# Kernel tuning notes

Hardware: AMD Instinct MI355X
Metric: run time of the kernel (lower is better)

Reference implementation:

```python
import jax, jax.numpy as jnp
import numpy as np

N_NODES = 100_000
N_EDGES = 1_600_000
N_GRAPHS = 64
EPS = 1e-7  # GENConv message epsilon
D_IN, D_H, D_OUT, OUT_DIM = 128, 192, 128, 10


def _w(k, fan_in, fan_out):
    return jax.random.normal(k, (fan_in, fan_out), jnp.float32) * (1.0 / np.sqrt(fan_in))


def setup_inputs() -> dict:
    key = jax.random.key(0)
    ks = jax.random.split(key, 8)
    return {
        "x": jax.random.normal(ks[0], (N_NODES, D_IN), jnp.float32),
        "W0": _w(ks[1], D_IN, D_H), "b0": jnp.zeros((D_H,), jnp.float32),
        "W1": _w(ks[2], D_H, D_H), "b1": jnp.zeros((D_H,), jnp.float32),
        "W2": _w(ks[3], D_H, D_H), "b2": jnp.zeros((D_H,), jnp.float32),
        "W3": _w(ks[4], D_H, D_OUT), "b3": jnp.zeros((D_OUT,), jnp.float32),
        "Wfc": _w(ks[5], D_OUT, OUT_DIM), "bfc": jnp.zeros((OUT_DIM,), jnp.float32),
        "edge_index": jax.random.randint(ks[6], (2, N_EDGES), 0, N_NODES, jnp.int32),
        "batch": jnp.sort(jax.random.randint(ks[7], (N_NODES,), 0, N_GRAPHS, jnp.int32)),
    }


def _genconv(x, W, b, src, dst):
    # GENConv (num_layers=1, aggr='add'): message = relu(x_j) + eps,
    # scatter-add to dst, residual add, single Linear MLP.
    msg = jax.nn.relu(x[src]) + EPS          # [E, d]
    agg = jax.ops.segment_sum(msg, dst, num_segments=N_NODES)  # [N, d]
    return (x + agg) @ W + b


def reference(x, W0, b0, W1, b1, W2, b2, W3, b3, Wfc, bfc, edge_index, batch):
    src, dst = edge_index[0], edge_index[1]  # source_to_target flow
    for W, b in ((W0, b0), (W1, b1), (W2, b2), (W3, b3)):
        x = _genconv(x, W, b, src, dst)
    # global mean pool over graphs
    sums = jax.ops.segment_sum(x, batch, num_segments=N_GRAPHS)
    counts = jax.ops.segment_sum(jnp.ones((x.shape[0],), x.dtype), batch,
                                 num_segments=N_GRAPHS)
    pooled = sums / jnp.maximum(counts, 1.0)[:, None]  # [G, D_OUT]
    logits = pooled @ Wfc + bfc                        # [G, OUT_DIM]
    return jax.nn.log_softmax(logits, axis=1)
```

## Files before the change

kernel.cpp:

```cpp
#include <hip/hip_runtime.h>
#include <hip/hip_bf16.h>
#include <stdint.h>

constexpr int NN = 100000;
constexpr int NE = 1600000;
constexpr int NG = 64;
constexpr int S  = 192;
constexpr int NB_SCAN = 98;
constexpr unsigned int ZOFF = (unsigned int)NN * 384u;

constexpr int PREP_CONVX_BLK = 12500;
constexpr int PREP_INDEG_BLK = 1563;
constexpr int PREP_CONVW_BLK = 384;
constexpr int PREP_GB_BLK    = 391;
constexpr int PREP_GRID = PREP_CONVX_BLK + PREP_INDEG_BLK + PREP_CONVW_BLK + PREP_GB_BLK;

constexpr int EG_BLOCKS = 391;
constexpr int HROW = 50048;
constexpr int QROW = HROW / 4;

typedef __bf16 bf16x8 __attribute__((ext_vector_type(8)));
typedef float  f32x16 __attribute__((ext_vector_type(16)));
typedef float  f32x2  __attribute__((ext_vector_type(2)));

union U16x4 { uint4 u; bf16x8 b; };

__device__ __forceinline__ float bl(unsigned int u) { return __uint_as_float(u << 16); }
__device__ __forceinline__ float bh(unsigned int u) { return __uint_as_float(u & 0xffff0000u); }
__device__ __forceinline__ float b16f(unsigned short u) { return __uint_as_float(((unsigned int)u) << 16); }
__device__ __forceinline__ unsigned int fb(float f) {
    unsigned int u = __float_as_uint(f);
    return (u + 0x7fffu + ((u >> 16) & 1u)) >> 16;
}
__device__ __forceinline__ unsigned int prelu(unsigned int u) {
    unsigned int r;
    asm("v_pk_max_f16 %0, %1, %2" : "=v"(r) : "v"(u), "v"(0u));
    return r;
}
__device__ __forceinline__ unsigned int cnt2bf(unsigned int h) {
    float f0 = (float)(h & 0xffffu);
    float f1 = (float)(h >> 16);
    return (__float_as_uint(f0) >> 16) | (__float_as_uint(f1) & 0xffff0000u);
}

__global__ __launch_bounds__(256) void k_prep(const float* __restrict__ x,
                                              const int* __restrict__ ei,
                                              const int* __restrict__ bat,
                                              const float* __restrict__ W0, const float* __restrict__ W1,
                                              const float* __restrict__ W2,
                                              unsigned short* __restrict__ A_,
                                              int* __restrict__ indeg, int* __restrict__ slot,
                                              unsigned short* __restrict__ T0, unsigned short* __restrict__ T1,
                                              unsigned short* __restrict__ T2,
                                              int* __restrict__ nstart) {
    const int b = blockIdx.x;
    if (b < PREP_CONVX_BLK) {
        int id = b * 256 + threadIdx.x;
        if (id < 96) ((unsigned int*)(A_ + (size_t)NN * S))[id] = 0u;
        int row = id >> 5, c4 = id & 31;
        float4 v = ((const float4*)x)[id];
        uint2 a;
        a.x = fb(v.x) | (fb(v.y) << 16);
        a.y = fb(v.z) | (fb(v.w) << 16);
        *(uint2*)(A_ + row * S + c4 * 4) = a;
    } else if (b < PREP_CONVX_BLK + PREP_INDEG_BLK) {
        int e4 = ((b - PREP_CONVX_BLK) * 256 + threadIdx.x) * 4;
        if (e4 < NE) {
            int4 d = *(const int4*)(ei + NE + e4);
            int4 sl;
            sl.x = atomicAdd(&indeg[d.x], 1);
            sl.y = atomicAdd(&indeg[d.y], 1);
            sl.z = atomicAdd(&indeg[d.z], 1);
            sl.w = atomicAdd(&indeg[d.w], 1);
            *(int4*)(slot + e4) = sl;
        }
    } else if (b < PREP_CONVX_BLK + PREP_INDEG_BLK + PREP_CONVW_BLK) {
        int id = (b - PREP_CONVX_BLK - PREP_INDEG_BLK) * 256 + threadIdx.x;
        const float* W; unsigned short* T; int N, base;
        if      (id < 24576) { W = W0; T = T0; N = 192; base = 0;     }
        else if (id < 61440) { W = W1; T = T1; N = 192; base = 24576; }
        else                 { W = W2; T = T2; N = 192; base = 61440; }
        int lid = id - base;
        int ci = lid >> 3, j = lid & 7;
        int kc = ci / N, n = ci % N;
        T[lid] = (unsigned short)fb(W[(kc * 8 + j) * N + n]);
    } else {
        int n = (b - PREP_CONVX_BLK - PREP_INDEG_BLK - PREP_CONVW_BLK) * 256 + threadIdx.x;
        if (n < NN) {
            int b0 = bat[n];
            int bprev = (n == 0) ? -1 : bat[n - 1];
            for (int g = bprev + 1; g <= b0; g++) nstart[g] = n;
            if (n == NN - 1)
                for (int g = b0 + 1; g < NG; g++) nstart[g] = NN;
        }
    }
}

__global__ __launch_bounds__(1024) void k_scan1(const int* __restrict__ indeg, int* __restrict__ offs,
                                                int* __restrict__ partials) {
    __shared__ int s[1024];
    int t = threadIdx.x;
    int gid = blockIdx.x * 1024 + t;
    int v = (gid < NN) ? indeg[gid] : 0;
    s[t] = v;
    __syncthreads();
    for (int d = 1; d < 1024; d <<= 1) {
        int tv = (t >= d) ? s[t - d] : 0;
        __syncthreads();
        s[t] += tv;
        __syncthreads();
    }
    if (gid < NN) offs[gid + 1] = s[t];
    if (t == 1023) partials[blockIdx.x] = s[1023];
}

__global__ __launch_bounds__(128) void k_scan2(int* __restrict__ offs, int* __restrict__ partials) {
    __shared__ int s[128];
    int t = threadIdx.x;
    int v = (t < NB_SCAN) ? partials[t] : 0;
    s[t] = v;
    __syncthreads();
    for (int d = 1; d < 128; d <<= 1) {
        int tv = (t >= d) ? s[t - d] : 0;
        __syncthreads();
        s[t] += tv;
        __syncthreads();
    }
    if (t < NB_SCAN) partials[t] = s[t] - v;
    if (t == 0) offs[0] = 0;
}

__device__ __forceinline__ int toff(const int* __restrict__ offs, const int* __restrict__ part, int j) {
    return j ? (offs[j] + part[(j - 1) >> 10]) : 0;
}

__global__ __launch_bounds__(256) void k_fill(const int* __restrict__ ei, const int* __restrict__ offs,
                                              const int* __restrict__ part,
                                              const int* __restrict__ slot, int* __restrict__ csr) {
    int e4 = (blockIdx.x * 256 + threadIdx.x) * 4;
    if (e4 >= NE) return;
    int4 sv = *(const int4*)(ei + e4);
    int4 dv = *(const int4*)(ei + NE + e4);
    int4 sl = *(const int4*)(slot + e4);
    csr[toff(offs, part, dv.x) + sl.x] = sv.x;
    csr[toff(offs, part, dv.y) + sl.y] = sv.y;
    csr[toff(offs, part, dv.z) + sl.z] = sv.z;
    csr[toff(offs, part, dv.w) + sl.w] = sv.w;
}

__global__ __launch_bounds__(256, 8) void k_agg192(const unsigned short* __restrict__ Ain,
                                                   unsigned short* __restrict__ Yout,
                                                   const int* __restrict__ offs,
                                                   const int* __restrict__ part,
                                                   const int* __restrict__ indeg,
                                                   const int* __restrict__ csr) {
    const int w = threadIdx.x >> 6, lane = threadIdx.x & 63;
    const int i = __builtin_amdgcn_readfirstlane(blockIdx.x * 4 + w);
    const bool act = lane < 48;
    const int deg   = __builtin_amdgcn_readfirstlane(indeg[i]);
    const int start = __builtin_amdgcn_readfirstlane(toff(offs, part, i));
    const int fo = (act ? lane : 47) * 8;
    const char* Ab = (const char*)Ain;

    f32x2 A01, A23;
    {
        uint2 p = *(const uint2*)(Ab + (size_t)i * 384 + fo);
        const float ed = 1e-7f * (float)deg;
        A01 = (f32x2){bl(p.x) + ed, bh(p.x) + ed};
        A23 = (f32x2){bl(p.y) + ed, bh(p.y) + ed};
    }

    const int* ecsr = csr + start;
    for (int e = 0; e < deg; e += 16) {
        unsigned int off[16];
#pragma unroll
        for (int k = 0; k < 16; k++) {
            int v = ecsr[e + k];
            off[k] = (e + k < deg) ? (unsigned int)v * 384u : ZOFF;
        }
        uint2 p[16];
#pragma unroll
        for (int k = 0; k < 16; k++)
            p[k] = *(const uint2*)(Ab + (size_t)off[k] + fo);
#pragma unroll
        for (int k = 0; k < 16; k++) {
            unsigned int rx = prelu(p[k].x), ry = prelu(p[k].y);
            A01 += (f32x2){bl(rx), bh(rx)};
            A23 += (f32x2){bl(ry), bh(ry)};
        }
    }
    if (act) {
        uint2 o;
        o.x = fb(A01.x) | (fb(A01.y) << 16);
        o.y = fb(A23.x) | (fb(A23.y) << 16);
        *(uint2*)(Yout + (size_t)i * S + lane * 4) = o;
    }
}

__global__ __launch_bounds__(256, 8) void k_agg128(const unsigned short* __restrict__ Ain,
                                                   unsigned short* __restrict__ Yout,
                                                   const int* __restrict__ offs,
                                                   const int* __restrict__ part,
                                                   const int* __restrict__ indeg,
                                                   const int* __restrict__ csr) {
    const int w = threadIdx.x >> 6, lane = threadIdx.x & 63;
    const int i = __builtin_amdgcn_readfirstlane(blockIdx.x * 4 + w);
    const int deg   = __builtin_amdgcn_readfirstlane(indeg[i]);
    const int start = __builtin_amdgcn_readfirstlane(toff(offs, part, i));
    const int fo = lane * 4;
    const char* Ab = (const char*)Ain;

    f32x2 A01;
    {
        unsigned int p = *(const unsigned int*)(Ab + (size_t)i * 384 + fo);
        const float ed = 1e-7f * (float)deg;
        A01 = (f32x2){bl(p) + ed, bh(p) + ed};
    }

    const int* ecsr = csr + start;
    for (int e = 0; e < deg; e += 16) {
        unsigned int off[16];
#pragma unroll
        for (int k = 0; k < 16; k++) {
            int v = ecsr[e + k];
            off[k] = (e + k < deg) ? (unsigned int)v * 384u : ZOFF;
        }
        unsigned int q[16];
#pragma unroll
        for (int k = 0; k < 16; k++)
            q[k] = *(const unsigned int*)(Ab + (size_t)off[k] + fo);
#pragma unroll
        for (int k = 0; k < 16; k++) {
            unsigned int r = prelu(q[k]);
            A01 += (f32x2){bl(r), bh(r)};
        }
    }
    *(unsigned int*)(Yout + (size_t)i * S + lane * 2) =
        fb(A01.x) | (fb(A01.y) << 16);
}

template <int K, int N>
__global__ __launch_bounds__(256) void k_gemm(const unsigned short* __restrict__ Yin,
                                              const unsigned short* __restrict__ WtC,
                                              const float* __restrict__ bias,
                                              unsigned short* __restrict__ Aout) {
    static_assert(K % 16 == 0 && N % 32 == 0, "");
    const int w = threadIdx.x >> 6, lane = threadIdx.x & 63;
    const int rt = blockIdx.x * 4 + w;
    if (rt >= (NN / 32)) return;
    const int hl = lane >> 5, lr = lane & 31;
    const int row0 = rt * 32;
    f32x16 acc[N / 32];
#pragma unroll
    for (int c = 0; c < N / 32; c++)
#pragma unroll
        for (int r = 0; r < 16; r++) acc[c][r] = 0.f;

    const unsigned short* ap = Yin + (row0 + lr) * S + hl * 8;
    const uint4* b4 = (const uint4*)WtC;
#pragma unroll
    for (int ks = 0; ks < K / 16; ks++) {
        U16x4 a;
        a.u = *(const uint4*)(ap + ks * 16);
#pragma unroll
        for (int c = 0; c < N / 32; c++) {
            U16x4 b;
            b.u = b4[(ks * 2 + hl) * N + c * 32 + lr];
            acc[c] = __builtin_amdgcn_mfma_f32_32x32x16_bf16(a.b, b.b, acc[c], 0, 0, 0);
        }
    }
#pragma unroll
    for (int c = 0; c < N / 32; c++) {
        const int col = c * 32 + lr;
        const float bc = bias[col];
#pragma unroll
        for (int r = 0; r < 16; r++) {
            const int row = row0 + (r & 3) + 8 * (r >> 2) + 4 * hl;
            Aout[row * S + col] = (unsigned short)fb(acc[c][r] + bc);
        }
    }
}

__global__ __launch_bounds__(256) void k_histpool(const int* __restrict__ csr,
                                                  const int* __restrict__ offs,
                                                  const int* __restrict__ part,
                                                  const int* __restrict__ nstart,
                                                  unsigned int* __restrict__ hist,
                                                  const unsigned short* __restrict__ X3,
                                                  const int* __restrict__ bat,
                                                  const int* __restrict__ indeg,
                                                  float* __restrict__ sums, float* __restrict__ cnt,
                                                  float* __restrict__ degsum) {
    const int b = blockIdx.x;
    if (b < 256) {
        const int g = b >> 2, q = b & 3;
        unsigned int* hrow = hist + (size_t)g * HROW;
        const unsigned int q0 = q * QROW;
        for (int i = threadIdx.x; i < QROW; i += 256) hrow[q0 + i] = 0u;
        __syncthreads();
        const int s0 = toff(offs, part, nstart[g]);
        const int s1 = (g == NG - 1) ? NE : toff(offs, part, nstart[g + 1]);
        for (int p = s0 + threadIdx.x; p < s1; p += 256) {
            int src = csr[p];
            unsigned int h = (unsigned int)src >> 1;
            if (h - q0 < (unsigned int)QROW)
                atomicAdd(&hrow[h], 1u << (16 * (src & 1)));
        }
    } else {
        const int pb = b - 256;
        const int f = threadIdx.x;
        if (f >= 192) return;
        int n0 = pb * 200;
        int n1 = min(n0 + 200, NN);
        int cur = bat[n0];
        float acc = 0.f;
        int run = 0, dacc = 0;
        for (int n = n0; n < n1; n++) {
            int g = bat[n];
            if (g != cur) {
                atomicAdd(&sums[cur * 192 + f], acc);
                if (f == 0) { atomicAdd(&cnt[cur], (float)run); atomicAdd(&degsum[cur], (float)dacc); }
                acc = 0.f; run = 0; dacc = 0; cur = g;
            }
            acc += b16f(X3[(size_t)n * S + f]);
            run++;
            if (f == 0) dacc += indeg[n];
        }
        atomicAdd(&sums[cur * 192 + f], acc);
        if (f == 0) { atomicAdd(&cnt[cur], (float)run); atomicAdd(&degsum[cur], (float)dacc); }
    }
}

__global__ __launch_bounds__(384) void k_egemm(const unsigned short* __restrict__ X3,
                                               const unsigned int* __restrict__ hist,
                                               float* __restrict__ partials) {
    const int wv = threadIdx.x >> 6, lane = threadIdx.x & 63;
    const int b = blockIdx.x;
    const int j0 = b * 256;
    const int hl = lane >> 5, lr = lane & 31;
    const int feat = wv * 32 + lr;
    f32x16 acc[2];
#pragma unroll
    for (int m = 0; m < 2; m++)
#pragma unroll
        for (int r = 0; r < 16; r++) acc[m][r] = 0.f;

    for (int kk = 0; kk < 16; kk++) {
        const int jh = (j0 >> 1) + kk * 8 + hl * 4;
        U16x4 af[2];
#pragma unroll
        for (int m = 0; m < 2; m++) {
            uint4 h = *(const uint4*)(hist + (size_t)(m * 32 + lr) * HROW + jh);
            af[m].u = (uint4){cnt2bf(h.x), cnt2bf(h.y), cnt2bf(h.z), cnt2bf(h.w)};
        }
        U16x4 bf;
#pragma unroll
        for (int tp = 0; tp < 4; tp++) {
            int je = j0 + kk * 16 + hl * 8 + tp * 2;
            int ja = min(je, NN), jb = min(je + 1, NN);
            unsigned int u0 = X3[(size_t)ja * S + feat];
            unsigned int u1 = X3[(size_t)jb * S + feat];
            ((unsigned int*)&bf.u)[tp] = prelu(u0 | (u1 << 16));
        }
#pragma unroll
        for (int m = 0; m < 2; m++)
            acc[m] = __builtin_amdgcn_mfma_f32_32x32x16_bf16(af[m].b, bf.b, acc[m], 0, 0, 0);
    }
    float* pb = partials + (size_t)b * 12288;
#pragma unroll
    for (int m = 0; m < 2; m++)
#pragma unroll
        for (int r = 0; r < 16; r++) {
            const int g = m * 32 + (r & 3) + 8 * (r >> 2) + 4 * hl;
            pb[g * 192 + feat] = acc[m][r];
        }
}

__global__ __launch_bounds__(256) void k_reduce(const float* __restrict__ partials,
                                                float* __restrict__ msg) {
    int gf = blockIdx.x * 256 + threadIdx.x;
    if (gf >= 12288) return;
    float s = 0.f;
    for (int p = 0; p < EG_BLOCKS; p++)
        s += partials[(size_t)p * 12288 + gf];
    msg[gf] = s;
}

__global__ __launch_bounds__(128) void k_head(const float* __restrict__ sums, const float* __restrict__ msg,
                                              const float* __restrict__ cnt, const float* __restrict__ degsum,
                                              const float* __restrict__ W3, const float* __restrict__ b3,
                                              const float* __restrict__ Wfc, const float* __restrict__ bfc,
                                              float* __restrict__ out) {
    __shared__ float py[192];
    __shared__ float tl[128];
    __shared__ float lg[10];
    const int g = blockIdx.x, t = threadIdx.x;
    const float inv = 1.f / fmaxf(cnt[g], 1.f);
    const float ed = 1e-7f * degsum[g];
    for (int k = t; k < 192; k += 128)
        py[k] = (sums[g * 192 + k] + msg[g * 192 + k] + ed) * inv;
    __syncthreads();
    float tf = b3[t];
    for (int k = 0; k < 192; k++) tf += py[k] * W3[k * 128 + t];
    tl[t] = tf;
    __syncthreads();
    if (t < 10) {
        float s = bfc[t];
        for (int f = 0; f < 128; f++) s += tl[f] * Wfc[f * 10 + t];
        lg[t] = s;
    }
    __syncthreads();
    if (t < 10) {
        float m = lg[0];
        for (int k = 1; k < 10; k++) m = fmaxf(m, lg[k]);
        float se = 0.f;
        for (int k = 0; k < 10; k++) se += expf(lg[k] - m);
        out[g * 10 + t] = lg[t] - m - logf(se);
    }
}

constexpr size_t A0_OFF     = 0;
constexpr size_t A1_OFF     = 38400384;
constexpr size_t HIST_REL   = 0;
constexpr size_t PARTS_REL  = 12812288;
constexpr size_t CSR_OFF    = 76800384;
constexpr size_t OFFS_OFF   = 83200384;
constexpr size_t INDEG_OFF  = 83600512;
constexpr size_t SUMS_OFF   = 84000512;
constexpr size_t CNT_OFF    = 84049664;
constexpr size_t DEGS_OFF   = 84049920;
constexpr size_t PART_OFF   = 84050176;
constexpr size_t NSTART_OFF = 84050688;
constexpr size_t WT0_OFF    = 84050944;
constexpr size_t WT1_OFF    = 84100096;
constexpr size_t WT2_OFF    = 84173824;
constexpr size_t MSG_OFF    = 84247552;

extern "C" void kernel_launch(void* const* d_in, const int* in_sizes, int n_in,
                              void* d_out, int out_size, void* d_ws, size_t ws_size,
                              hipStream_t stream) {
    const float* x   = (const float*)d_in[0];
    const float* W0  = (const float*)d_in[1];
    const float* b0  = (const float*)d_in[2];
    const float* W1  = (const float*)d_in[3];
    const float* b1  = (const float*)d_in[4];
    const float* W2  = (const float*)d_in[5];
    const float* b2  = (const float*)d_in[6];
    const float* W3  = (const float*)d_in[7];
    const float* b3  = (const float*)d_in[8];
    const float* Wfc = (const float*)d_in[9];
    const float* bfc = (const float*)d_in[10];
    const int*   ei  = (const int*)d_in[11];
    const int*   bat = (const int*)d_in[12];
    float* out = (float*)d_out;

    char* ws = (char*)d_ws;
    unsigned short* A0  = (unsigned short*)(ws + A0_OFF);
    unsigned short* A1  = (unsigned short*)(ws + A1_OFF);
    int* slot   = (int*)(ws + A1_OFF);
    unsigned int* hist  = (unsigned int*)(ws + A1_OFF + HIST_REL);
    float* parts        = (float*)(ws + A1_OFF + PARTS_REL);
    int* csr    = (int*)(ws + CSR_OFF);
    int* offs   = (int*)(ws + OFFS_OFF);
    int* indeg  = (int*)(ws + INDEG_OFF);
    int* part   = (int*)(ws + PART_OFF);
    int* nstart = (int*)(ws + NSTART_OFF);
    unsigned short* Wt0 = (unsigned short*)(ws + WT0_OFF);
    unsigned short* Wt1 = (unsigned short*)(ws + WT1_OFF);
    unsigned short* Wt2 = (unsigned short*)(ws + WT2_OFF);
    float* sums   = (float*)(ws + SUMS_OFF);
    float* cnt    = (float*)(ws + CNT_OFF);
    float* degsum = (float*)(ws + DEGS_OFF);
    float* msg    = (float*)(ws + MSG_OFF);

    hipMemsetAsync(ws + INDEG_OFF, 0, 449664, stream);

    k_prep<<<PREP_GRID, 256, 0, stream>>>(x, ei, bat, W0, W1, W2, A0, indeg, slot,
                                          Wt0, Wt1, Wt2, nstart);

    k_scan1<<<NB_SCAN, 1024, 0, stream>>>(indeg, offs, part);
    k_scan2<<<1, 128, 0, stream>>>(offs, part);
    k_fill<<<(NE / 4 + 255) / 256, 256, 0, stream>>>(ei, offs, part, slot, csr);

    const int AGG_GRID  = NN / 4;
    const int GEMM_GRID = (NN / 32 + 3) / 4;

    k_agg128<<<AGG_GRID, 256, 0, stream>>>(A0, A1, offs, part, indeg, csr);
    k_gemm<128, 192><<<GEMM_GRID, 256, 0, stream>>>(A1, Wt0, b0, A0);
    k_agg192<<<AGG_GRID, 256, 0, stream>>>(A0, A1, offs, part, indeg, csr);
    k_gemm<192, 192><<<GEMM_GRID, 256, 0, stream>>>(A1, Wt1, b1, A0);
    k_agg192<<<AGG_GRID, 256, 0, stream>>>(A0, A1, offs, part, indeg, csr);
    k_gemm<192, 192><<<GEMM_GRID, 256, 0, stream>>>(A1, Wt2, b2, A0);

    k_histpool<<<756, 256, 0, stream>>>(csr, offs, part, nstart, hist, A0, bat, indeg,
                                        sums, cnt, degsum);
    k_egemm<<<EG_BLOCKS, 384, 0, stream>>>(A0, hist, parts);
    k_reduce<<<48, 256, 0, stream>>>(parts, msg);
    k_head<<<NG, 128, 0, stream>>>(sums, msg, cnt, degsum, W3, b3, Wfc, bfc, out);
}
```

Before: 671.2 us.

## Fuse partial reduction into head, rebalance histogram and pool work, widen indeg atomics

```diff
diff --git a/kernel.cpp b/kernel.cpp
--- a/kernel.cpp
+++ b/kernel.cpp
@@ -10,14 +10,13 @@
 constexpr unsigned int ZOFF = (unsigned int)NN * 384u;
 
 constexpr int PREP_CONVX_BLK = 12500;
-constexpr int PREP_INDEG_BLK = 1563;
+constexpr int PREP_INDEG_BLK = 391;
 constexpr int PREP_CONVW_BLK = 384;
 constexpr int PREP_GB_BLK    = 391;
 constexpr int PREP_GRID = PREP_CONVX_BLK + PREP_INDEG_BLK + PREP_CONVW_BLK + PREP_GB_BLK;
 
 constexpr int EG_BLOCKS = 391;
 constexpr int HROW = 50048;
-constexpr int QROW = HROW / 4;
 
 typedef __bf16 bf16x8 __attribute__((ext_vector_type(8)));
 typedef float  f32x16 __attribute__((ext_vector_type(16)));
@@ -64,15 +63,30 @@
         a.y = fb(v.z) | (fb(v.w) << 16);
         *(uint2*)(A_ + row * S + c4 * 4) = a;
     } else if (b < PREP_CONVX_BLK + PREP_INDEG_BLK) {
-        int e4 = ((b - PREP_CONVX_BLK) * 256 + threadIdx.x) * 4;
-        if (e4 < NE) {
-            int4 d = *(const int4*)(ei + NE + e4);
-            int4 sl;
-            sl.x = atomicAdd(&indeg[d.x], 1);
-            sl.y = atomicAdd(&indeg[d.y], 1);
-            sl.z = atomicAdd(&indeg[d.z], 1);
-            sl.w = atomicAdd(&indeg[d.w], 1);
-            *(int4*)(slot + e4) = sl;
+        int id = (b - PREP_CONVX_BLK) * 256 + threadIdx.x;
+        int e16 = id * 16;
+        if (e16 < NE) {
+            const int4* dp = (const int4*)(ei + NE + e16);
+            int4 d0 = dp[0], d1 = dp[1], d2 = dp[2], d3 = dp[3];
+            int4 s0, s1, s2, s3;
+            s0.x = atomicAdd(&indeg[d0.x], 1);
+            s0.y = atomicAdd(&indeg[d0.y], 1);
+            s0.z = atomicAdd(&indeg[d0.z], 1);
+            s0.w = atomicAdd(&indeg[d0.w], 1);
+            s1.x = atomicAdd(&indeg[d1.x], 1);
+            s1.y = atomicAdd(&indeg[d1.y], 1);
+            s1.z = atomicAdd(&indeg[d1.z], 1);
+            s1.w = atomicAdd(&indeg[d1.w], 1);
+            s2.x = atomicAdd(&indeg[d2.x], 1);
+            s2.y = atomicAdd(&indeg[d2.y], 1);
+            s2.z = atomicAdd(&indeg[d2.z], 1);
+            s2.w = atomicAdd(&indeg[d2.w], 1);
+            s3.x = atomicAdd(&indeg[d3.x], 1);
+            s3.y = atomicAdd(&indeg[d3.y], 1);
+            s3.z = atomicAdd(&indeg[d3.z], 1);
+            s3.w = atomicAdd(&indeg[d3.w], 1);
+            int4* sp = (int4*)(slot + e16);
+            sp[0] = s0; sp[1] = s1; sp[2] = s2; sp[3] = s3;
         }
     } else if (b < PREP_CONVX_BLK + PREP_INDEG_BLK + PREP_CONVW_BLK) {
         int id = (b - PREP_CONVX_BLK - PREP_INDEG_BLK) * 256 + threadIdx.x;
@@ -294,24 +308,22 @@
     const int b = blockIdx.x;
     if (b < 256) {
         const int g = b >> 2, q = b & 3;
-        unsigned int* hrow = hist + (size_t)g * HROW;
-        const unsigned int q0 = q * QROW;
-        for (int i = threadIdx.x; i < QROW; i += 256) hrow[q0 + i] = 0u;
-        __syncthreads();
         const int s0 = toff(offs, part, nstart[g]);
         const int s1 = (g == NG - 1) ? NE : toff(offs, part, nstart[g + 1]);
-        for (int p = s0 + threadIdx.x; p < s1; p += 256) {
+        const int len = s1 - s0;
+        const int qs = s0 + (int)(((long long)len * q) >> 2);
+        const int qe = s0 + (int)(((long long)len * (q + 1)) >> 2);
+        unsigned int* hrow = hist + (size_t)g * HROW;
+        for (int p = qs + threadIdx.x; p < qe; p += 256) {
             int src = csr[p];
-            unsigned int h = (unsigned int)src >> 1;
-            if (h - q0 < (unsigned int)QROW)
-                atomicAdd(&hrow[h], 1u << (16 * (src & 1)));
+            atomicAdd(&hrow[(unsigned int)src >> 1], 1u << (16 * (src & 1)));
         }
     } else {
         const int pb = b - 256;
         const int f = threadIdx.x;
         if (f >= 192) return;
-        int n0 = pb * 200;
-        int n1 = min(n0 + 200, NN);
+        int n0 = pb * 50;
+        int n1 = min(n0 + 50, NN);
         int cur = bat[n0];
         float acc = 0.f;
         int run = 0, dacc = 0;
@@ -376,17 +388,8 @@
         }
 }
 
-__global__ __launch_bounds__(256) void k_reduce(const float* __restrict__ partials,
-                                                float* __restrict__ msg) {
-    int gf = blockIdx.x * 256 + threadIdx.x;
-    if (gf >= 12288) return;
-    float s = 0.f;
-    for (int p = 0; p < EG_BLOCKS; p++)
-        s += partials[(size_t)p * 12288 + gf];
-    msg[gf] = s;
-}
-
-__global__ __launch_bounds__(128) void k_head(const float* __restrict__ sums, const float* __restrict__ msg,
+__global__ __launch_bounds__(192) void k_head(const float* __restrict__ sums,
+                                              const float* __restrict__ partials,
                                               const float* __restrict__ cnt, const float* __restrict__ degsum,
                                               const float* __restrict__ W3, const float* __restrict__ b3,
                                               const float* __restrict__ Wfc, const float* __restrict__ bfc,
@@ -397,12 +400,23 @@
     const int g = blockIdx.x, t = threadIdx.x;
     const float inv = 1.f / fmaxf(cnt[g], 1.f);
     const float ed = 1e-7f * degsum[g];
-    for (int k = t; k < 192; k += 128)
-        py[k] = (sums[g * 192 + k] + msg[g * 192 + k] + ed) * inv;
+    const float* pp = partials + g * 192 + t;
+    float s0 = 0.f, s1 = 0.f, s2 = 0.f, s3 = 0.f;
+    int p = 0;
+    for (; p + 4 <= EG_BLOCKS; p += 4) {
+        s0 += pp[(size_t)(p + 0) * 12288];
+        s1 += pp[(size_t)(p + 1) * 12288];
+        s2 += pp[(size_t)(p + 2) * 12288];
+        s3 += pp[(size_t)(p + 3) * 12288];
+    }
+    for (; p < EG_BLOCKS; p++) s0 += pp[(size_t)p * 12288];
+    py[t] = (sums[g * 192 + t] + ((s0 + s1) + (s2 + s3)) + ed) * inv;
     __syncthreads();
-    float tf = b3[t];
-    for (int k = 0; k < 192; k++) tf += py[k] * W3[k * 128 + t];
-    tl[t] = tf;
+    if (t < 128) {
+        float tf = b3[t];
+        for (int k = 0; k < 192; k++) tf += py[k] * W3[k * 128 + t];
+        tl[t] = tf;
+    }
     __syncthreads();
     if (t < 10) {
         float s = bfc[t];
@@ -434,7 +448,6 @@
 constexpr size_t WT0_OFF    = 84050944;
 constexpr size_t WT1_OFF    = 84100096;
 constexpr size_t WT2_OFF    = 84173824;
-constexpr size_t MSG_OFF    = 84247552;
 
 extern "C" void kernel_launch(void* const* d_in, const int* in_sizes, int n_in,
                               void* d_out, int out_size, void* d_ws, size_t ws_size,
@@ -471,7 +484,6 @@
     float* sums   = (float*)(ws + SUMS_OFF);
     float* cnt    = (float*)(ws + CNT_OFF);
     float* degsum = (float*)(ws + DEGS_OFF);
-    float* msg    = (float*)(ws + MSG_OFF);
 
     hipMemsetAsync(ws + INDEG_OFF, 0, 449664, stream);
 
@@ -492,9 +504,9 @@
     k_agg192<<<AGG_GRID, 256, 0, stream>>>(A0, A1, offs, part, indeg, csr);
     k_gemm<192, 192><<<GEMM_GRID, 256, 0, stream>>>(A1, Wt2, b2, A0);
 
-    k_histpool<<<756, 256, 0, stream>>>(csr, offs, part, nstart, hist, A0, bat, indeg,
-                                        sums, cnt, degsum);
+    hipMemsetAsync(ws + A1_OFF + HIST_REL, 0, 12812288, stream);
+    k_histpool<<<2256, 256, 0, stream>>>(csr, offs, part, nstart, hist, A0, bat, indeg,
+                                         sums, cnt, degsum);
     k_egemm<<<EG_BLOCKS, 384, 0, stream>>>(A0, hist, parts);
-    k_reduce<<<48, 256, 0, stream>>>(parts, msg);
-    k_head<<<NG, 128, 0, stream>>>(sums, msg, cnt, degsum, W3, b3, Wfc, bfc, out);
-}
+    k_head<<<NG, 192, 0, stream>>>(sums, parts, cnt, degsum, W3, b3, Wfc, bfc, out);
+}
```

New measurement: 672.0 us. Within noise of the previous version (+0.1%).
